# Kernel optimization log

Hardware: AMD Instinct MI355X
Metric: run time of the kernel (lower is better)

Reference implementation:

```python
import jax, jax.numpy as jnp
import numpy as np

PROB_THRESHOLD = 0.5
SCALE_FACTOR = 0.1


def _dist_matrix(mask, prob_threshold):
    """Exact squared Euclidean distance transform to nearest pixel with
    mask > prob_threshold (faithful to RMNet's dist_matrix.forward).
    mask: [B, H, W] float. Returns [B, H, W] float squared distances
    (0 at foreground pixels, large finite value if no foreground exists).
    """
    B, H, W = mask.shape
    fg = mask > prob_threshold
    BIG = jnp.float32(H * H + W * W)  # sentinel > any real distance

    # --- vertical pass: L1 distance along rows to nearest fg in same column ---
    row = jnp.arange(H, dtype=jnp.float32)[None, :, None]  # [1,H,1]
    # nearest fg at-or-above: row - (running max of fg row indices)
    up = row - jax.lax.cummax(jnp.where(fg, row, -BIG), axis=1)
    # nearest fg at-or-below: (running min of fg row indices from below) - row
    neg = jnp.where(fg, -row, -BIG)
    down = -jnp.flip(jax.lax.cummax(jnp.flip(neg, axis=1), axis=1), axis=1) - row
    d_vert = jnp.minimum(jnp.minimum(up, down), BIG)  # [B,H,W]
    g2 = d_vert * d_vert  # squared vertical distance

    # --- horizontal pass: D[i,j] = min_j' ( g2[i,j'] + (j-j')^2 ) (exact EDT) ---
    col = jnp.arange(W, dtype=jnp.float32)
    sq = (col[:, None] - col[None, :]) ** 2  # [W(j), W(j')]
    # [B,H,1,W] + [W,W] -> [B,H,W,W] -> min over j'
    dist_sq = jnp.min(g2[:, :, None, :] + sq[None, None, :, :], axis=-1)
    return dist_sq


def setup_inputs() -> dict:
    key = jax.random.key(0)
    mask = jax.random.uniform(key, (8, 192, 192), dtype=jnp.float32)
    return {"mask": mask}


def reference(mask) -> jnp.ndarray:
    dist_sq = _dist_matrix(mask, PROB_THRESHOLD)
    dist = jnp.sqrt(dist_sq) * SCALE_FACTOR
    return jax.nn.sigmoid(-dist) * 2.0
```

## Files before the change

kernel.cpp:

```cpp
#include <hip/hip_runtime.h>
#include <math.h>

namespace {
constexpr int B = 8, H = 192, W = 192;
constexpr float BIGF = 73728.0f;
constexpr int BAND = 16;
constexpr int RWIN = 4;
constexpr int RESC = 16;
constexpr int NT   = 768;
constexpr int WP   = W + 2 * RESC;
}

__global__ void __launch_bounds__(NT) dm_fused(const float* __restrict__ mask,
                                               float* __restrict__ out) {
    __shared__ unsigned long long colbits[3][W];
    __shared__ float g2p[BAND][WP];

    const int b    = blockIdx.x & 7;
    const int band = blockIdx.x >> 3;
    const int i0   = band * BAND;
    const int tid  = threadIdx.x;

    if (tid < 3 * W) {
        const int w  = tid / W;
        const int jj = tid - w * W;
        const float* p = mask + ((size_t)b * H + w * 64) * W + jj;
        unsigned long long v0 = 0, v1 = 0, v2 = 0, v3 = 0;
        #pragma unroll
        for (int k = 0; k < 16; ++k) {
            v0 |= (unsigned long long)(p[(size_t)k * W]        > 0.5f) << k;
            v1 |= (unsigned long long)(p[(size_t)(k + 16) * W] > 0.5f) << k;
            v2 |= (unsigned long long)(p[(size_t)(k + 32) * W] > 0.5f) << k;
            v3 |= (unsigned long long)(p[(size_t)(k + 48) * W] > 0.5f) << k;
        }
        colbits[w][jj] = v0 | (v1 << 16) | (v2 << 32) | (v3 << 48);
    } else {
        const int t = tid - 3 * W;
        for (int s = t; s < BAND * 2 * RESC; s += 192) {
            const int r = s >> 5;
            const int c = s & 31;
            const int idx = (c < RESC) ? c : (W + RESC + (c - RESC));
            g2p[r][idx] = 1e30f;
        }
    }
    __syncthreads();

    const int j  = tid % W;
    const int ig = tid / W;
    const unsigned long long lo  = colbits[0][j];
    const unsigned long long mid = colbits[1][j];
    const unsigned long long hi  = colbits[2][j];

    #pragma unroll
    for (int rr = 0; rr < BAND / 4; ++rr) {
        const int i = i0 + rr * 4 + ig;

        const int wdi = i >> 6, r = i & 63;
        const unsigned long long mle = (2ULL << r) - 1ULL;
        const unsigned long long mge = ~((1ULL << r) - 1ULL);
        unsigned long long a0 = (wdi == 0) ? (lo & mle) : lo;
        unsigned long long a1 = (wdi == 0) ? 0ULL : ((wdi == 1) ? (mid & mle) : mid);
        unsigned long long a2 = (wdi == 2) ? (hi & mle) : 0ULL;
        unsigned long long c0 = (wdi == 0) ? (lo & mge) : 0ULL;
        unsigned long long c1 = (wdi == 1) ? (mid & mge) : ((wdi == 0) ? mid : 0ULL);
        unsigned long long c2 = (wdi == 2) ? (hi & mge) : hi;

        int hidx = a2 ? (191 - __clzll((long long)a2))
                 : (a1 ? (127 - __clzll((long long)a1))
                 : (a0 ? (63 - __clzll((long long)a0)) : -1));
        int lidx = c0 ? (__ffsll((unsigned long long)c0) - 1)
                 : (c1 ? (63 + __ffsll((unsigned long long)c1))
                 : (c2 ? (127 + __ffsll((unsigned long long)c2)) : -1));

        const float fi   = (float)i;
        const float up   = (hidx >= 0) ? (fi - (float)hidx) : (fi + BIGF);
        const float down = (lidx >= 0) ? ((float)lidx - fi) : (BIGF - fi);
        const float d = fminf(fminf(up, down), BIGF);
        g2p[rr * 4 + ig][RESC + j] = d * d;
    }
    __syncthreads();

    const float fj = (float)j;
    #pragma unroll
    for (int rr = 0; rr < BAND / 4; ++rr) {
        const int row = rr * 4 + ig;
        const float* rowp = &g2p[row][RESC + j];
        float best = rowp[0];
        #pragma unroll
        for (int dj = 1; dj <= RWIN; ++dj) {
            const float c = (float)(dj * dj);
            best = fminf(best, rowp[dj]  + c);
            best = fminf(best, rowp[-dj] + c);
        }
        if (__any(best > (float)(RWIN * RWIN))) {
            #pragma unroll
            for (int dj = RWIN + 1; dj <= RESC; ++dj) {
                const float c = (float)(dj * dj);
                best = fminf(best, rowp[dj]  + c);
                best = fminf(best, rowp[-dj] + c);
            }
            if (__any(best > (float)(RESC * RESC))) {
                for (int jp = 0; jp < W; ++jp) {
                    const float diff = fj - (float)jp;
                    best = fminf(best, fmaf(diff, diff, g2p[row][RESC + jp]));
                }
            }
        }

        const float dist = sqrtf(best) * 0.1f;
        out[((size_t)b * H + (i0 + row)) * W + j] = __fdividef(2.0f, 1.0f + __expf(dist));
    }
}

extern "C" void kernel_launch(void* const* d_in, const int* in_sizes, int n_in,
                              void* d_out, int out_size, void* d_ws, size_t ws_size,
                              hipStream_t stream) {
    const float* mask = (const float*)d_in[0];
    float* out = (float*)d_out;
    dm_fused<<<B * (H / BAND), NT, 0, stream>>>(mask, out);
}
```

Measured before the change: 10.53 us.

## Vectorize mask loads with float4 and compute four output columns per thread

The mask bit-packing now uses float4 loads, with each thread covering 4 columns over 16 rows and storing 16-bit chunks that are later gathered into per-column 64-bit words. The horizontal pass gives each thread 4 adjacent columns: it loads a 12-wide register window via float4 LDS reads, reuses it across the 4 outputs, and writes results with a float4 store. The intent is fewer global and LDS transactions and shared neighbour reuse. In exchange the threads per column shrink and the divergent fallback path does 4x work per thread.

Result: faster. 10.31 us (-2.0%).

```diff
diff --git a/kernel.cpp b/kernel.cpp
--- a/kernel.cpp
+++ b/kernel.cpp
@@ -13,7 +13,7 @@
 
 __global__ void __launch_bounds__(NT) dm_fused(const float* __restrict__ mask,
                                                float* __restrict__ out) {
-    __shared__ unsigned long long colbits[3][W];
+    __shared__ unsigned long long chunk64[12][48];
     __shared__ float g2p[BAND][WP];
 
     const int b    = blockIdx.x & 7;
@@ -21,21 +21,25 @@
     const int i0   = band * BAND;
     const int tid  = threadIdx.x;
 
-    if (tid < 3 * W) {
-        const int w  = tid / W;
-        const int jj = tid - w * W;
-        const float* p = mask + ((size_t)b * H + w * 64) * W + jj;
-        unsigned long long v0 = 0, v1 = 0, v2 = 0, v3 = 0;
+    if (tid < 576) {
+        const int wq = tid / 48;
+        const int g  = tid - wq * 48;
+        const float4* p = (const float4*)(mask + ((size_t)b * H + wq * 16) * W) + g;
+        unsigned int v0 = 0, v1 = 0, v2 = 0, v3 = 0;
         #pragma unroll
         for (int k = 0; k < 16; ++k) {
-            v0 |= (unsigned long long)(p[(size_t)k * W]        > 0.5f) << k;
-            v1 |= (unsigned long long)(p[(size_t)(k + 16) * W] > 0.5f) << k;
-            v2 |= (unsigned long long)(p[(size_t)(k + 32) * W] > 0.5f) << k;
-            v3 |= (unsigned long long)(p[(size_t)(k + 48) * W] > 0.5f) << k;
+            const float4 m = p[(size_t)k * (W / 4)];
+            v0 |= (m.x > 0.5f ? 1u : 0u) << k;
+            v1 |= (m.y > 0.5f ? 1u : 0u) << k;
+            v2 |= (m.z > 0.5f ? 1u : 0u) << k;
+            v3 |= (m.w > 0.5f ? 1u : 0u) << k;
         }
-        colbits[w][jj] = v0 | (v1 << 16) | (v2 << 32) | (v3 << 48);
+        chunk64[wq][g] = (unsigned long long)v0
+                       | ((unsigned long long)v1 << 16)
+                       | ((unsigned long long)v2 << 32)
+                       | ((unsigned long long)v3 << 48);
     } else {
-        const int t = tid - 3 * W;
+        const int t = tid - 576;
         for (int s = t; s < BAND * 2 * RESC; s += 192) {
             const int r = s >> 5;
             const int c = s & 31;
@@ -45,70 +49,110 @@
     }
     __syncthreads();
 
-    const int j  = tid % W;
-    const int ig = tid / W;
-    const unsigned long long lo  = colbits[0][j];
-    const unsigned long long mid = colbits[1][j];
-    const unsigned long long hi  = colbits[2][j];
+    {
+        const int j  = tid % W;
+        const int ig = tid / W;
+        const unsigned short* c16 = (const unsigned short*)chunk64;
+        unsigned long long lo = 0, mid = 0, hi = 0;
+        #pragma unroll
+        for (int wq = 0; wq < 4; ++wq) lo  |= (unsigned long long)c16[wq * 192 + j]       << (16 * wq);
+        #pragma unroll
+        for (int wq = 0; wq < 4; ++wq) mid |= (unsigned long long)c16[(4 + wq) * 192 + j] << (16 * wq);
+        #pragma unroll
+        for (int wq = 0; wq < 4; ++wq) hi  |= (unsigned long long)c16[(8 + wq) * 192 + j] << (16 * wq);
 
-    #pragma unroll
-    for (int rr = 0; rr < BAND / 4; ++rr) {
-        const int i = i0 + rr * 4 + ig;
+        #pragma unroll
+        for (int rr = 0; rr < BAND / 4; ++rr) {
+            const int i = i0 + rr * 4 + ig;
+            const int wdi = i >> 6, r = i & 63;
+            const unsigned long long mle = (2ULL << r) - 1ULL;
+            const unsigned long long mge = ~((1ULL << r) - 1ULL);
+            unsigned long long a0 = (wdi == 0) ? (lo & mle) : lo;
+            unsigned long long a1 = (wdi == 0) ? 0ULL : ((wdi == 1) ? (mid & mle) : mid);
+            unsigned long long a2 = (wdi == 2) ? (hi & mle) : 0ULL;
+            unsigned long long c0 = (wdi == 0) ? (lo & mge) : 0ULL;
+            unsigned long long c1 = (wdi == 1) ? (mid & mge) : ((wdi == 0) ? mid : 0ULL);
+            unsigned long long c2 = (wdi == 2) ? (hi & mge) : hi;
 
-        const int wdi = i >> 6, r = i & 63;
-        const unsigned long long mle = (2ULL << r) - 1ULL;
-        const unsigned long long mge = ~((1ULL << r) - 1ULL);
-        unsigned long long a0 = (wdi == 0) ? (lo & mle) : lo;
-        unsigned long long a1 = (wdi == 0) ? 0ULL : ((wdi == 1) ? (mid & mle) : mid);
-        unsigned long long a2 = (wdi == 2) ? (hi & mle) : 0ULL;
-        unsigned long long c0 = (wdi == 0) ? (lo & mge) : 0ULL;
-        unsigned long long c1 = (wdi == 1) ? (mid & mge) : ((wdi == 0) ? mid : 0ULL);
-        unsigned long long c2 = (wdi == 2) ? (hi & mge) : hi;
+            int hidx = a2 ? (191 - __clzll((long long)a2))
+                     : (a1 ? (127 - __clzll((long long)a1))
+                     : (a0 ? (63 - __clzll((long long)a0)) : -1));
+            int lidx = c0 ? (__ffsll((unsigned long long)c0) - 1)
+                     : (c1 ? (63 + __ffsll((unsigned long long)c1))
+                     : (c2 ? (127 + __ffsll((unsigned long long)c2)) : -1));
 
-        int hidx = a2 ? (191 - __clzll((long long)a2))
-                 : (a1 ? (127 - __clzll((long long)a1))
-                 : (a0 ? (63 - __clzll((long long)a0)) : -1));
-        int lidx = c0 ? (__ffsll((unsigned long long)c0) - 1)
-                 : (c1 ? (63 + __ffsll((unsigned long long)c1))
-                 : (c2 ? (127 + __ffsll((unsigned long long)c2)) : -1));
-
-        const float fi   = (float)i;
-        const float up   = (hidx >= 0) ? (fi - (float)hidx) : (fi + BIGF);
-        const float down = (lidx >= 0) ? ((float)lidx - fi) : (BIGF - fi);
-        const float d = fminf(fminf(up, down), BIGF);
-        g2p[rr * 4 + ig][RESC + j] = d * d;
+            const float fi   = (float)i;
+            const float up   = (hidx >= 0) ? (fi - (float)hidx) : (fi + BIGF);
+            const float down = (lidx >= 0) ? ((float)lidx - fi) : (BIGF - fi);
+            const float d = fminf(fminf(up, down), BIGF);
+            g2p[rr * 4 + ig][RESC + j] = d * d;
+        }
     }
     __syncthreads();
 
-    const float fj = (float)j;
-    #pragma unroll
-    for (int rr = 0; rr < BAND / 4; ++rr) {
-        const int row = rr * 4 + ig;
-        const float* rowp = &g2p[row][RESC + j];
-        float best = rowp[0];
+    {
+        const int rloc  = tid / 48;
+        const int g     = tid - rloc * 48;
+        const int jbase = 4 * g;
+        const float* rowbase = &g2p[rloc][RESC + jbase];
+
+        float t[12];
+        const float4 w0 = *(const float4*)(rowbase - 4);
+        const float4 w1 = *(const float4*)(rowbase);
+        const float4 w2 = *(const float4*)(rowbase + 4);
+        t[0] = w0.x; t[1] = w0.y; t[2]  = w0.z; t[3]  = w0.w;
+        t[4] = w1.x; t[5] = w1.y; t[6]  = w1.z; t[7]  = w1.w;
+        t[8] = w2.x; t[9] = w2.y; t[10] = w2.z; t[11] = w2.w;
+
+        float best[4];
         #pragma unroll
-        for (int dj = 1; dj <= RWIN; ++dj) {
-            const float c = (float)(dj * dj);
-            best = fminf(best, rowp[dj]  + c);
-            best = fminf(best, rowp[-dj] + c);
+        for (int c = 0; c < 4; ++c) {
+            float bst = t[c + 4];
+            #pragma unroll
+            for (int dj = 1; dj <= RWIN; ++dj) {
+                const float cc = (float)(dj * dj);
+                bst = fminf(bst, t[c + 4 + dj] + cc);
+                bst = fminf(bst, t[c + 4 - dj] + cc);
+            }
+            best[c] = bst;
         }
-        if (__any(best > (float)(RWIN * RWIN))) {
+
+        float mx = fmaxf(fmaxf(best[0], best[1]), fmaxf(best[2], best[3]));
+        if (__any(mx > (float)(RWIN * RWIN))) {
             #pragma unroll
-            for (int dj = RWIN + 1; dj <= RESC; ++dj) {
-                const float c = (float)(dj * dj);
-                best = fminf(best, rowp[dj]  + c);
-                best = fminf(best, rowp[-dj] + c);
+            for (int c = 0; c < 4; ++c) {
+                #pragma unroll
+                for (int dj = RWIN + 1; dj <= RESC; ++dj) {
+                    const float cc = (float)(dj * dj);
+                    best[c] = fminf(best[c], rowbase[c + dj] + cc);
+                    best[c] = fminf(best[c], rowbase[c - dj] + cc);
+                }
             }
-            if (__any(best > (float)(RESC * RESC))) {
+            mx = fmaxf(fmaxf(best[0], best[1]), fmaxf(best[2], best[3]));
+            if (__any(mx > (float)(RESC * RESC))) {
                 for (int jp = 0; jp < W; ++jp) {
-                    const float diff = fj - (float)jp;
-                    best = fminf(best, fmaf(diff, diff, g2p[row][RESC + jp]));
+                    const float gv = g2p[rloc][RESC + jp];
+                    #pragma unroll
+                    for (int c = 0; c < 4; ++c) {
+                        const float diff = (float)(jbase + c) - (float)jp;
+                        best[c] = fminf(best[c], fmaf(diff, diff, gv));
+                    }
                 }
             }
         }
 
-        const float dist = sqrtf(best) * 0.1f;
-        out[((size_t)b * H + (i0 + row)) * W + j] = __fdividef(2.0f, 1.0f + __expf(dist));
+        float4 o;
+        {
+            const float d0 = sqrtf(best[0]) * 0.1f;
+            const float d1 = sqrtf(best[1]) * 0.1f;
+            const float d2 = sqrtf(best[2]) * 0.1f;
+            const float d3 = sqrtf(best[3]) * 0.1f;
+            o.x = __fdividef(2.0f, 1.0f + __expf(d0));
+            o.y = __fdividef(2.0f, 1.0f + __expf(d1));
+            o.z = __fdividef(2.0f, 1.0f + __expf(d2));
+            o.w = __fdividef(2.0f, 1.0f + __expf(d3));
+        }
+        *(float4*)(out + ((size_t)b * H + (i0 + rloc)) * W + jbase) = o;
     }
 }
 
```
